# Optimization experiments

Measured on AMD Instinct MI355X. Metric: run time of the kernel, lower is better.

Reference implementation:

```python
import jax, jax.numpy as jnp
import numpy as np

D_MODEL, N_HEADS, D_FF = 1024, 16, 4096
SCALE = 0.1          # lookup-activation input quantization step
NUM_BITS = 8
LEVELS = 1 << NUM_BITS   # 256
HALF = LEVELS // 2       # 128
MAX_EXP = 4
EPS = 1e-5


def pow2_weight(key, shape, max_exp=MAX_EXP):
    """Ternary power-of-two weights: values in {0, +/-2^{-e}}, e in [max_exp, max_exp+3].
    Exponent range keeps fan-in-1024 outputs O(1)."""
    k1, k2 = jax.random.split(key)
    sign = jax.random.randint(k1, shape, -1, 2).astype(jnp.float32)  # {-1,0,1}
    e = jax.random.randint(k2, shape, max_exp, max_exp + 4).astype(jnp.float32)
    return sign * jnp.exp2(-e)


def setup_inputs() -> dict:
    key = jax.random.key(0)
    ks = jax.random.split(key, 8)
    x = jax.random.normal(ks[0], (4, 2048, D_MODEL), dtype=jnp.float32)
    return {
        "x": x,
        "ln1_g": jnp.ones((D_MODEL,), jnp.float32),
        "ln1_b": jnp.zeros((D_MODEL,), jnp.float32),
        "wq": pow2_weight(ks[1], (D_MODEL, D_MODEL)),
        "wk": pow2_weight(ks[2], (D_MODEL, D_MODEL)),
        "wv": pow2_weight(ks[3], (D_MODEL, D_MODEL)),
        "wo": pow2_weight(ks[4], (D_MODEL, D_MODEL)),
        "ln2_g": jnp.ones((D_MODEL,), jnp.float32),
        "ln2_b": jnp.zeros((D_MODEL,), jnp.float32),
        "w1": pow2_weight(ks[5], (D_MODEL, D_FF)),
        "w2": pow2_weight(ks[6], (D_FF, D_MODEL)),
    }


def _layernorm(x, g, b):
    mu = jnp.mean(x, axis=-1, keepdims=True)
    var = jnp.var(x, axis=-1, keepdims=True)
    return (x - mu) * jax.lax.rsqrt(var + EPS) * g + b


def _lookup_act(x):
    # StructuredLookupActivation: quantize input to 2^num_bits levels, gather from
    # a precomputed GELU table (proved via Lasso lookup in the SNARK).
    grid = (jnp.arange(LEVELS, dtype=jnp.float32) - HALF) * SCALE
    table = jax.nn.gelu(grid)
    idx = jnp.clip(jnp.round(x / SCALE).astype(jnp.int32) + HALF, 0, LEVELS - 1)
    return table[idx]


def _linear_attention(x, wq, wk, wv, wo):
    B, S, D = x.shape
    H, Dh = N_HEADS, D // N_HEADS
    q = (x @ wq).reshape(B, S, H, Dh)
    k = (x @ wk).reshape(B, S, H, Dh)
    v = (x @ wv).reshape(B, S, H, Dh)
    # elu+1 feature map -> O(S*Dh^2) linear attention (no [S,S] scores)
    phi_q = jax.nn.elu(q) + 1.0
    phi_k = jax.nn.elu(k) + 1.0
    kv = jnp.einsum('bshd,bshe->bhde', phi_k, v)          # [B,H,Dh,Dh]
    z = jnp.sum(phi_k, axis=1)                            # [B,H,Dh]
    num = jnp.einsum('bshd,bhde->bshe', phi_q, kv)        # [B,S,H,Dh]
    den = jnp.einsum('bshd,bhd->bsh', phi_q, z)[..., None] + 1e-6
    out = (num / den).reshape(B, S, D)
    return out @ wo


def reference(x, ln1_g, ln1_b, wq, wk, wv, wo, ln2_g, ln2_b, w1, w2):
    # norm -> linear attention -> residual
    x = x + _linear_attention(_layernorm(x, ln1_g, ln1_b), wq, wk, wv, wo)
    # norm -> ternary FFN with lookup activation -> residual
    h = _layernorm(x, ln2_g, ln2_b)
    x = x + (_lookup_act(h @ w1) @ w2)
    return x
```

## Files before the change

### kernel.cpp

```cpp
#include <hip/hip_runtime.h>
#include <cstdint>
#include <cstddef>


#define D_MODEL 1024
#define SEQ     2048
#define BATCH   4
#define NTOK    8192
#define NHEADS  16
#define DH      64
#define DFF     4096
#define KVCH    16
#define CHROWS  (SEQ / KVCH)
#define PSTRIDE 4160

typedef _Float16 half8 __attribute__((ext_vector_type(8)));
typedef float f32x4 __attribute__((ext_vector_type(4)));

__device__ __forceinline__ unsigned short f2h(float x) {
  _Float16 h = (_Float16)x;
  union { _Float16 h; unsigned short u; } c; c.h = h; return c.u;
}
__device__ __forceinline__ float h2f(unsigned short u) {
  union { unsigned short u; _Float16 h; } c; c.u = u; return (float)c.h;
}

__device__ __forceinline__ float phi_act(float x) {
  return x > 0.f ? x + 1.f : expf(x);
}

__device__ __forceinline__ float gelu_exact(float v) {
  float c = 0.7978845608028654f;
  float t = tanhf(c * (v + 0.044715f * v * v * v));
  return 0.5f * v * (1.f + t);
}

__device__ __forceinline__ int frow(int r) {
  return (r ^ (r >> 3)) & 7;
}

__device__ __forceinline__ void gl_lds16(const void* g, void* l) {
  __builtin_amdgcn_global_load_lds(
      (const __attribute__((address_space(1))) unsigned int*)g,
      (__attribute__((address_space(3))) unsigned int*)l, 16, 0, 0);
}

__global__ __launch_bounds__(256) void convT4(const float* __restrict__ W0,
                                              const float* __restrict__ W1,
                                              const float* __restrict__ W2,
                                              const float* __restrict__ W3,
                                              unsigned short* __restrict__ D0,
                                              unsigned short* __restrict__ D3) {
  __shared__ float tile[64][65];
  int zz = blockIdx.z;
  const float* W = zz == 0 ? W0 : zz == 1 ? W1 : zz == 2 ? W2 : W3;
  unsigned short* WT = zz < 3 ? (D0 + (size_t)zz * D_MODEL * D_MODEL) : D3;
  int kb = blockIdx.y << 6, nb = blockIdx.x << 6;
  int t = threadIdx.x;
  int rr = t >> 4, cc = (t & 15) << 2;
#pragma unroll
  for (int i = 0; i < 4; ++i) {
    int r = rr + (i << 4);
    float4 v = *(const float4*)(W + (size_t)(kb + r) * D_MODEL + nb + cc);
    tile[r][cc] = v.x; tile[r][cc + 1] = v.y; tile[r][cc + 2] = v.z; tile[r][cc + 3] = v.w;
  }
  __syncthreads();
#pragma unroll
  for (int i = 0; i < 4; ++i) {
    int n = rr + (i << 4);
    ushort4 o;
    o.x = f2h(tile[cc + 0][n]); o.y = f2h(tile[cc + 1][n]);
    o.z = f2h(tile[cc + 2][n]); o.w = f2h(tile[cc + 3][n]);
    *(ushort4*)(WT + (size_t)(nb + n) * D_MODEL + kb + cc) = o;
  }
}

__global__ __launch_bounds__(256) void convT(const float* __restrict__ W,
                                             unsigned short* __restrict__ WT,
                                             int K, int N) {
  __shared__ float tile[64][65];
  int kb = blockIdx.y << 6, nb = blockIdx.x << 6;
  int t = threadIdx.x;
  int rr = t >> 4, cc = (t & 15) << 2;
#pragma unroll
  for (int i = 0; i < 4; ++i) {
    int r = rr + (i << 4);
    float4 v = *(const float4*)(W + (size_t)(kb + r) * N + nb + cc);
    tile[r][cc] = v.x; tile[r][cc + 1] = v.y; tile[r][cc + 2] = v.z; tile[r][cc + 3] = v.w;
  }
  __syncthreads();
#pragma unroll
  for (int i = 0; i < 4; ++i) {
    int n = rr + (i << 4);
    ushort4 o;
    o.x = f2h(tile[cc + 0][n]); o.y = f2h(tile[cc + 1][n]);
    o.z = f2h(tile[cc + 2][n]); o.w = f2h(tile[cc + 3][n]);
    *(ushort4*)(WT + (size_t)(nb + n) * K + kb + cc) = o;
  }
}

__global__ __launch_bounds__(256) void ln_kernel(const float* __restrict__ X,
                                                 const float* __restrict__ g,
                                                 const float* __restrict__ b,
                                                 unsigned short* __restrict__ Y) {
  int tok = blockIdx.x;
  int t = threadIdx.x;
  const float4* xr = (const float4*)(X + (size_t)tok * D_MODEL);
  float4 v = xr[t];
  float s  = v.x + v.y + v.z + v.w;
  float s2 = v.x * v.x + v.y * v.y + v.z * v.z + v.w * v.w;
#pragma unroll
  for (int o = 32; o > 0; o >>= 1) {
    s  += __shfl_down(s, o);
    s2 += __shfl_down(s2, o);
  }
  __shared__ float red[8];
  __shared__ float mu_s, rs_s;
  int wid = t >> 6;
  if ((t & 63) == 0) { red[wid] = s; red[wid + 4] = s2; }
  __syncthreads();
  if (t == 0) {
    float ts  = red[0] + red[1] + red[2] + red[3];
    float ts2 = red[4] + red[5] + red[6] + red[7];
    float mu  = ts * (1.f / D_MODEL);
    float var = ts2 * (1.f / D_MODEL) - mu * mu;
    mu_s = mu;
    rs_s = rsqrtf(var + 1e-5f);
  }
  __syncthreads();
  float mu = mu_s, rs = rs_s;
  float4 gv = ((const float4*)g)[t];
  float4 bv = ((const float4*)b)[t];
  ushort4 hv;
  hv.x = f2h((v.x - mu) * rs * gv.x + bv.x);
  hv.y = f2h((v.y - mu) * rs * gv.y + bv.y);
  hv.z = f2h((v.z - mu) * rs * gv.z + bv.z);
  hv.w = f2h((v.w - mu) * rs * gv.w + bv.w);
  ((ushort4*)(Y + (size_t)tok * D_MODEL))[t] = hv;
}

template <int EP, int BK>
__global__ __launch_bounds__(256, (BK == 64) ? 4 : 2) void mfma_gemm(
    const unsigned short* __restrict__ A,
    const unsigned short* __restrict__ BT,
    void* Cv, const float* R, int N, int K) {
  constexpr int SEGS = BK / 8;
  constexpr int RPC  = 64 / SEGS;
  constexpr int NJ   = 32 / RPC;
  __shared__ unsigned short smem[2 * 128 * BK];
  __shared__ float gtab[EP == 3 ? 256 : 1];
  unsigned short* sA = smem;
  unsigned short* sB = smem + 128 * BK;

  int t = threadIdx.x;
  if (EP == 3) gtab[t & 255] = gelu_exact((float)((t & 255) - 128) * 0.1f);

  int bm, bn;
  {
    int L = blockIdx.y * gridDim.x + blockIdx.x;
    if ((gridDim.y & 7) == 0) {
      int xcd = L & 7, wi = L >> 3;
      int mPerX = gridDim.y >> 3;
      bm = xcd * mPerX + wi / gridDim.x;
      bn = wi % gridDim.x;
    } else {
      bn = blockIdx.x; bm = blockIdx.y;
    }
  }

  int w = t >> 6, l = t & 63;
  int lrow = l / SEGS;
  int lseg = l & (SEGS - 1);
  int m0 = bm << 7;
  int n0 = bn << 7;
  size_t strideB = (size_t)K * 2;

  const char* gA[NJ]; const char* gB[NJ];
  int ldsOff[NJ];
#pragma unroll
  for (int j = 0; j < NJ; ++j) {
    int row = (w << 5) + j * RPC + lrow;
    int gso = (lseg ^ frow(row)) << 4;
    gA[j] = (const char*)A + (size_t)(m0 + row) * strideB + gso;
    gB[j] = (const char*)BT + (size_t)(n0 + row) * strideB + gso;
    ldsOff[j] = ((w << 5) + j * RPC) * BK;
  }

  int wm = w >> 1, wn = w & 1;
  int m16 = l & 15, qd = l >> 4;

  f32x4 acc[4][4];
#pragma unroll
  for (int i = 0; i < 4; ++i)
#pragma unroll
    for (int j = 0; j < 4; ++j) acc[i][j] = (f32x4){0.f, 0.f, 0.f, 0.f};

  for (int k0 = 0; k0 < K; k0 += BK) {
    size_t kb = (size_t)k0 * 2;
#pragma unroll
    for (int j = 0; j < NJ; ++j) {
      gl_lds16(gA[j] + kb, sA + ldsOff[j]);
      gl_lds16(gB[j] + kb, sB + ldsOff[j]);
    }
    __syncthreads();
#pragma unroll
    for (int kk = 0; kk < BK / 32; ++kk) {
      int ksb = (kk << 2) + qd;
      half8 af[4], bf[4];
#pragma unroll
      for (int mt = 0; mt < 4; ++mt) {
        int r = (wm << 6) + (mt << 4) + m16;
        int slot = ksb ^ frow(r);
        af[mt] = *(const half8*)(sA + r * BK + (slot << 3));
      }
#pragma unroll
      for (int nt = 0; nt < 4; ++nt) {
        int r = (wn << 6) + (nt << 4) + m16;
        int slot = ksb ^ frow(r);
        bf[nt] = *(const half8*)(sB + r * BK + (slot << 3));
      }
#pragma unroll
      for (int mt = 0; mt < 4; ++mt)
#pragma unroll
        for (int nt = 0; nt < 4; ++nt)
          acc[mt][nt] = __builtin_amdgcn_mfma_f32_16x16x32_f16(af[mt], bf[nt], acc[mt][nt], 0, 0, 0);
    }
    __syncthreads();
  }

  int sel = n0 >> 10;
  size_t slab = (size_t)sel * ((size_t)NTOK * D_MODEL);
  int colL = (n0 & 1023) + (wn << 6) + m16;

  int colBase = n0 + (wn << 6) + m16;
#pragma unroll
  for (int mt = 0; mt < 4; ++mt) {
    int rBase = m0 + (wm << 6) + (mt << 4) + (qd << 2);
#pragma unroll
    for (int nt = 0; nt < 4; ++nt) {
      int col = colBase + (nt << 4);
#pragma unroll
      for (int i = 0; i < 4; ++i) {
        float v = acc[mt][nt][i];
        if (EP == 4) {
          if (sel < 2) v = phi_act(v);
          size_t idx = slab + (size_t)(rBase + i) * D_MODEL + colL + (nt << 4);
          ((unsigned short*)Cv)[idx] = f2h(v);
        } else {
          size_t idx = (size_t)(rBase + i) * N + col;
          if (EP == 2)      ((float*)Cv)[idx] = R[idx] + v;
          else if (EP == 3) {
            float r = rintf(v / 0.1f);
            int iq = (int)r + 128;
            iq = iq < 0 ? 0 : (iq > 255 ? 255 : iq);
            ((unsigned short*)Cv)[idx] = f2h(gtab[iq]);
          } else          ((float*)Cv)[idx] = v;
        }
      }
    }
  }
}

__global__ __launch_bounds__(256) void kvz_partial(const unsigned short* __restrict__ PK,
                                                   const unsigned short* __restrict__ V,
                                                   float* __restrict__ P) {
  int c = blockIdx.x, bh = blockIdx.y;
  int b = bh >> 4, h = bh & 15;
  __shared__ float pk[8][64];
  __shared__ float vv[8][64];
  int t = threadIdx.x;
  const size_t base = ((size_t)b * SEQ + (size_t)c * CHROWS) * D_MODEL + h * DH;
  int u = t & 127;
  int lrow = u >> 4;
  int lcol = (u & 15) << 2;
  bool isV = (t >= 128);
  const unsigned short* src = isV ? V : PK;
  int dkb = (t >> 4) << 2;
  int deb = (t & 15) << 2;
  float acc[4][4] = {};
  float zacc = 0.f;
  for (int s0 = 0; s0 < CHROWS; s0 += 8) {
    ushort4 ld = *(const ushort4*)(src + base + (size_t)(s0 + lrow) * D_MODEL + lcol);
    float f0 = h2f(ld.x), f1 = h2f(ld.y), f2 = h2f(ld.z), f3 = h2f(ld.w);
    __syncthreads();
    if (isV) { vv[lrow][lcol] = f0; vv[lrow][lcol+1] = f1; vv[lrow][lcol+2] = f2; vv[lrow][lcol+3] = f3; }
    else     { pk[lrow][lcol] = f0; pk[lrow][lcol+1] = f1; pk[lrow][lcol+2] = f2; pk[lrow][lcol+3] = f3; }
    __syncthreads();
#pragma unroll
    for (int ss = 0; ss < 8; ++ss) {
      float4 a  = *(const float4*)&pk[ss][dkb];
      float4 bb = *(const float4*)&vv[ss][deb];
      acc[0][0] += a.x * bb.x; acc[0][1] += a.x * bb.y; acc[0][2] += a.x * bb.z; acc[0][3] += a.x * bb.w;
      acc[1][0] += a.y * bb.x; acc[1][1] += a.y * bb.y; acc[1][2] += a.y * bb.z; acc[1][3] += a.y * bb.w;
      acc[2][0] += a.z * bb.x; acc[2][1] += a.z * bb.y; acc[2][2] += a.z * bb.z; acc[2][3] += a.z * bb.w;
      acc[3][0] += a.w * bb.x; acc[3][1] += a.w * bb.y; acc[3][2] += a.w * bb.z; acc[3][3] += a.w * bb.w;
    }
    if (t < 64) {
#pragma unroll
      for (int ss = 0; ss < 8; ++ss) zacc += pk[ss][t];
    }
  }
  float* Pb = P + ((size_t)c * 64 + bh) * PSTRIDE;
#pragma unroll
  for (int i = 0; i < 4; ++i) {
    float4 o; o.x = acc[i][0]; o.y = acc[i][1]; o.z = acc[i][2]; o.w = acc[i][3];
    *(float4*)(Pb + (size_t)(dkb + i) * DH + deb) = o;
  }
  if (t < 64) Pb[4096 + t] = zacc;
}

__global__ __launch_bounds__(256) void kvz_reduce(const float* __restrict__ P,
                                                  float* __restrict__ KV,
                                                  float* __restrict__ Z) {
  int bh = blockIdx.x;
  int t = threadIdx.x;
  for (int i = t; i < PSTRIDE; i += 256) {
    float s = 0.f;
#pragma unroll
    for (int c = 0; c < KVCH; ++c)
      s += P[((size_t)c * 64 + bh) * PSTRIDE + i];
    if (i < 4096) KV[(size_t)bh * 4096 + i] = s;
    else          Z[(size_t)bh * 64 + (i - 4096)] = s;
  }
}

__global__ __launch_bounds__(256) void attn_kernel(const unsigned short* __restrict__ PQ,
                                                   const float* __restrict__ KVm,
                                                   const float* __restrict__ Z,
                                                   unsigned short* __restrict__ O) {
  int s0 = blockIdx.x << 6;
  int h = blockIdx.y, b = blockIdx.z;
  __shared__ float Pqt[64][64];
  __shared__ float Kv[64][64];
  __shared__ float den[64];
  __shared__ float zsh[64];
  int t = threadIdx.x;
  size_t qbase  = ((size_t)b * SEQ + s0) * D_MODEL + h * DH;
  size_t kvbase = (size_t)(b * NHEADS + h) * (DH * DH);
  int r0 = t >> 4;
  int c4 = (t & 15) << 2;
#pragma unroll
  for (int rr = 0; rr < 4; ++rr) {
    int row = r0 + (rr << 4);
    *(float4*)&Kv[row][c4] = *(const float4*)(KVm + kvbase + (size_t)row * DH + c4);
    ushort4 q = *(const ushort4*)(PQ + qbase + (size_t)row * D_MODEL + c4);
    Pqt[c4 + 0][row] = h2f(q.x);
    Pqt[c4 + 1][row] = h2f(q.y);
    Pqt[c4 + 2][row] = h2f(q.z);
    Pqt[c4 + 3][row] = h2f(q.w);
  }
  if (t < 16) *(float4*)&zsh[t << 2] = *(const float4*)(Z + (size_t)(b * NHEADS + h) * DH + (t << 2));
  __syncthreads();
  if (t < 64) {
    float d_ = 1e-6f;
#pragma unroll
    for (int dd = 0; dd < 64; ++dd) d_ += Pqt[dd][t] * zsh[dd];
    den[t] = d_;
  }
  __syncthreads();
  int tokb = (t >> 4) << 2, eb = (t & 15) << 2;
  float acc[4][4] = {};
#pragma unroll 8
  for (int dd = 0; dd < 64; ++dd) {
    float4 a  = *(const float4*)&Pqt[dd][tokb];
    float4 bb = *(const float4*)&Kv[dd][eb];
    acc[0][0] += a.x * bb.x; acc[0][1] += a.x * bb.y; acc[0][2] += a.x * bb.z; acc[0][3] += a.x * bb.w;
    acc[1][0] += a.y * bb.x; acc[1][1] += a.y * bb.y; acc[1][2] += a.y * bb.z; acc[1][3] += a.y * bb.w;
    acc[2][0] += a.z * bb.x; acc[2][1] += a.z * bb.y; acc[2][2] += a.z * bb.z; acc[2][3] += a.z * bb.w;
    acc[3][0] += a.w * bb.x; acc[3][1] += a.w * bb.y; acc[3][2] += a.w * bb.z; acc[3][3] += a.w * bb.w;
  }
#pragma unroll
  for (int i = 0; i < 4; ++i) {
    float dv = den[tokb + i];
    ushort4 hv;
    hv.x = f2h(acc[i][0] / dv);
    hv.y = f2h(acc[i][1] / dv);
    hv.z = f2h(acc[i][2] / dv);
    hv.w = f2h(acc[i][3] / dv);
    size_t oidx = ((size_t)b * SEQ + s0 + tokb + i) * D_MODEL + h * DH + eb;
    *(ushort4*)(O + oidx) = hv;
  }
}

extern "C" void kernel_launch(void* const* d_in, const int* in_sizes, int n_in,
                              void* d_out, int out_size, void* d_ws, size_t ws_size,
                              hipStream_t stream) {
  const float* x    = (const float*)d_in[0];
  const float* ln1g = (const float*)d_in[1];
  const float* ln1b = (const float*)d_in[2];
  const float* wq   = (const float*)d_in[3];
  const float* wk   = (const float*)d_in[4];
  const float* wv   = (const float*)d_in[5];
  const float* wo   = (const float*)d_in[6];
  const float* ln2g = (const float*)d_in[7];
  const float* ln2b = (const float*)d_in[8];
  const float* w1   = (const float*)d_in[9];
  const float* w2   = (const float*)d_in[10];
  float* out = (float*)d_out;
  char* ws = (char*)d_ws;

  const size_t MB = 1024 * 1024;
  unsigned short* xn   = (unsigned short*)(ws);
  unsigned short* qkv  = (unsigned short*)(ws + 32 * MB);
  unsigned short* phiq = qkv;
  unsigned short* phik = qkv + (size_t)NTOK * D_MODEL;
  unsigned short* vbuf = qkv + 2 * (size_t)NTOK * D_MODEL;
  unsigned short* ffn  = (unsigned short*)(ws + 32 * MB);
  unsigned short* w1T  = (unsigned short*)(ws + 96 * MB);
  unsigned short* w2T  = (unsigned short*)(ws + 104 * MB);
  unsigned short* woT  = (unsigned short*)(ws + 128 * MB);

  unsigned short* wqkvT = (unsigned short*)d_out;
  float* kvP = (float*)((char*)d_out + 6 * MB);
  float* kv  = (float*)((char*)d_out + 24 * MB);
  float* z   = (float*)((char*)d_out + 25 * MB);

  dim3 blk(256);

  convT4<<<dim3(D_MODEL / 64, D_MODEL / 64, 4), blk, 0, stream>>>(
      wq, wk, wv, wo, wqkvT, woT);

  ln_kernel<<<NTOK, blk, 0, stream>>>(x, ln1g, ln1b, xn);

  dim3 gQKV(3 * D_MODEL / 128, NTOK / 128);
  mfma_gemm<4, 64><<<gQKV, blk, 0, stream>>>(xn, wqkvT, qkv, nullptr, 3 * D_MODEL, D_MODEL);

  kvz_partial<<<dim3(KVCH, BATCH * NHEADS), blk, 0, stream>>>(phik, vbuf, kvP);
  kvz_reduce<<<BATCH * NHEADS, blk, 0, stream>>>(kvP, kv, z);

  attn_kernel<<<dim3(SEQ / 64, NHEADS, BATCH), blk, 0, stream>>>(phiq, kv, z, xn);

  convT<<<dim3(DFF / 64, D_MODEL / 64), blk, 0, stream>>>(w1, w1T, D_MODEL, DFF);
  convT<<<dim3(D_MODEL / 64, DFF / 64), blk, 0, stream>>>(w2, w2T, DFF, D_MODEL);

  dim3 gD(D_MODEL / 128, NTOK / 128);
  mfma_gemm<2, 128><<<gD, blk, 0, stream>>>(xn, woT, out, x, D_MODEL, D_MODEL);

  ln_kernel<<<NTOK, blk, 0, stream>>>(out, ln2g, ln2b, xn);

  dim3 gF(DFF / 128, NTOK / 128);
  mfma_gemm<3, 64><<<gF, blk, 0, stream>>>(xn, w1T, ffn, nullptr, DFF, D_MODEL);

  mfma_gemm<2, 128><<<gD, blk, 0, stream>>>(ffn, w2T, out, out, D_MODEL, DFF);
}
```

Baseline: 459.9 us.

## Double-buffer LDS in N=1024 GEMMs with BK=64 and simpler swizzle

The GEMM template now fixes BK at 64 and adds an optional double-buffered LDS pipeline, so the next K-tile's global-to-LDS load is issued before computing the current tile. The pipeline is used for the out-projection and FFN-down GEMMs, which have fewer blocks. The XOR swizzle changes from (r^(r>>3))&7 to r&7, and launch bounds for the single-buffered GEMMs drop from 4 to 2 waves per SIMD hint. Double-buffering halves the sync count per K step but doubles LDS use, and the simpler swizzle may change bank-conflict behaviour.

After: 472.4 us. 1.03x slower.

```diff
diff --git a/kernel.cpp b/kernel.cpp
--- a/kernel.cpp
+++ b/kernel.cpp
@@ -33,10 +33,6 @@
   float c = 0.7978845608028654f;
   float t = tanhf(c * (v + 0.044715f * v * v * v));
   return 0.5f * v * (1.f + t);
-}
-
-__device__ __forceinline__ int frow(int r) {
-  return (r ^ (r >> 3)) & 7;
 }
 
 __device__ __forceinline__ void gl_lds16(const void* g, void* l) {
@@ -139,18 +135,14 @@
   ((ushort4*)(Y + (size_t)tok * D_MODEL))[t] = hv;
 }
 
-template <int EP, int BK>
-__global__ __launch_bounds__(256, (BK == 64) ? 4 : 2) void mfma_gemm(
+template <int EP, bool DB>
+__global__ __launch_bounds__(256, 2) void mfma_gemm(
     const unsigned short* __restrict__ A,
     const unsigned short* __restrict__ BT,
     void* Cv, const float* R, int N, int K) {
-  constexpr int SEGS = BK / 8;
-  constexpr int RPC  = 64 / SEGS;
-  constexpr int NJ   = 32 / RPC;
-  __shared__ unsigned short smem[2 * 128 * BK];
+  constexpr int BK = 64;
+  __shared__ unsigned short smem[(DB ? 4 : 2) * 128 * BK];
   __shared__ float gtab[EP == 3 ? 256 : 1];
-  unsigned short* sA = smem;
-  unsigned short* sB = smem + 128 * BK;
 
   int t = threadIdx.x;
   if (EP == 3) gtab[t & 255] = gelu_exact((float)((t & 255) - 128) * 0.1f);
@@ -169,21 +161,21 @@
   }
 
   int w = t >> 6, l = t & 63;
-  int lrow = l / SEGS;
-  int lseg = l & (SEGS - 1);
+  int lrow = l >> 3;
+  int lseg = l & 7;
   int m0 = bm << 7;
   int n0 = bn << 7;
   size_t strideB = (size_t)K * 2;
 
-  const char* gA[NJ]; const char* gB[NJ];
-  int ldsOff[NJ];
-#pragma unroll
-  for (int j = 0; j < NJ; ++j) {
-    int row = (w << 5) + j * RPC + lrow;
-    int gso = (lseg ^ frow(row)) << 4;
+  const char* gA[4]; const char* gB[4];
+  int ldsOff[4];
+#pragma unroll
+  for (int j = 0; j < 4; ++j) {
+    int row = (w << 5) + (j << 3) + lrow;
+    int gso = (lseg ^ (row & 7)) << 4;
     gA[j] = (const char*)A + (size_t)(m0 + row) * strideB + gso;
     gB[j] = (const char*)BT + (size_t)(n0 + row) * strideB + gso;
-    ldsOff[j] = ((w << 5) + j * RPC) * BK;
+    ldsOff[j] = ((w << 5) + (j << 3)) * BK;
   }
 
   int wm = w >> 1, wn = w & 1;
@@ -195,28 +187,33 @@
 #pragma unroll
     for (int j = 0; j < 4; ++j) acc[i][j] = (f32x4){0.f, 0.f, 0.f, 0.f};
 
-  for (int k0 = 0; k0 < K; k0 += BK) {
-    size_t kb = (size_t)k0 * 2;
-#pragma unroll
-    for (int j = 0; j < NJ; ++j) {
-      gl_lds16(gA[j] + kb, sA + ldsOff[j]);
-      gl_lds16(gB[j] + kb, sB + ldsOff[j]);
-    }
-    __syncthreads();
-#pragma unroll
-    for (int kk = 0; kk < BK / 32; ++kk) {
+  auto stage = [&](int buf, size_t kb) {
+    unsigned short* dA = smem + buf * (2 * 128 * BK);
+    unsigned short* dB = dA + 128 * BK;
+#pragma unroll
+    for (int j = 0; j < 4; ++j) {
+      gl_lds16(gA[j] + kb, dA + ldsOff[j]);
+      gl_lds16(gB[j] + kb, dB + ldsOff[j]);
+    }
+  };
+
+  auto compute = [&](int buf) {
+    const unsigned short* sA = smem + buf * (DB ? 2 * 128 * BK : 0);
+    const unsigned short* sB = sA + 128 * BK;
+#pragma unroll
+    for (int kk = 0; kk < 2; ++kk) {
       int ksb = (kk << 2) + qd;
       half8 af[4], bf[4];
 #pragma unroll
       for (int mt = 0; mt < 4; ++mt) {
         int r = (wm << 6) + (mt << 4) + m16;
-        int slot = ksb ^ frow(r);
+        int slot = ksb ^ (r & 7);
         af[mt] = *(const half8*)(sA + r * BK + (slot << 3));
       }
 #pragma unroll
       for (int nt = 0; nt < 4; ++nt) {
         int r = (wn << 6) + (nt << 4) + m16;
-        int slot = ksb ^ frow(r);
+        int slot = ksb ^ (r & 7);
         bf[nt] = *(const half8*)(sB + r * BK + (slot << 3));
       }
 #pragma unroll
@@ -225,7 +222,25 @@
         for (int nt = 0; nt < 4; ++nt)
           acc[mt][nt] = __builtin_amdgcn_mfma_f32_16x16x32_f16(af[mt], bf[nt], acc[mt][nt], 0, 0, 0);
     }
+  };
+
+  if (DB) {
+    stage(0, 0);
     __syncthreads();
+    int nIter = K / BK;
+    for (int it = 0; it < nIter; ++it) {
+      int cur = it & 1;
+      if (it + 1 < nIter) stage(cur ^ 1, (size_t)(it + 1) * BK * 2);
+      compute(cur);
+      __syncthreads();
+    }
+  } else {
+    for (int k0 = 0; k0 < K; k0 += BK) {
+      stage(0, (size_t)k0 * 2);
+      __syncthreads();
+      compute(0);
+      __syncthreads();
+    }
   }
 
   int sel = n0 >> 10;
@@ -423,7 +438,7 @@
   ln_kernel<<<NTOK, blk, 0, stream>>>(x, ln1g, ln1b, xn);
 
   dim3 gQKV(3 * D_MODEL / 128, NTOK / 128);
-  mfma_gemm<4, 64><<<gQKV, blk, 0, stream>>>(xn, wqkvT, qkv, nullptr, 3 * D_MODEL, D_MODEL);
+  mfma_gemm<4, false><<<gQKV, blk, 0, stream>>>(xn, wqkvT, qkv, nullptr, 3 * D_MODEL, D_MODEL);
 
   kvz_partial<<<dim3(KVCH, BATCH * NHEADS), blk, 0, stream>>>(phik, vbuf, kvP);
   kvz_reduce<<<BATCH * NHEADS, blk, 0, stream>>>(kvP, kv, z);
@@ -434,12 +449,12 @@
   convT<<<dim3(D_MODEL / 64, DFF / 64), blk, 0, stream>>>(w2, w2T, DFF, D_MODEL);
 
   dim3 gD(D_MODEL / 128, NTOK / 128);
-  mfma_gemm<2, 128><<<gD, blk, 0, stream>>>(xn, woT, out, x, D_MODEL, D_MODEL);
+  mfma_gemm<2, true><<<gD, blk, 0, stream>>>(xn, woT, out, x, D_MODEL, D_MODEL);
 
   ln_kernel<<<NTOK, blk, 0, stream>>>(out, ln2g, ln2b, xn);
 
   dim3 gF(DFF / 128, NTOK / 128);
-  mfma_gemm<3, 64><<<gF, blk, 0, stream>>>(xn, w1T, ffn, nullptr, DFF, D_MODEL);
-
-  mfma_gemm<2, 128><<<gD, blk, 0, stream>>>(ffn, w2T, out, out, D_MODEL, DFF);
-}
+  mfma_gemm<3, false><<<gF, blk, 0, stream>>>(xn, w1T, ffn, nullptr, DFF, D_MODEL);
+
+  mfma_gemm<2, true><<<gD, blk, 0, stream>>>(ffn, w2T, out, out, D_MODEL, DFF);
+}
```
